# Kernel tuning notes

Hardware: AMD Instinct MI355X
Metric: run time of the kernel (lower is better)

The kernel has to match this reference:

```python
import jax, jax.numpy as jnp
import numpy as np

K = 10
ALPHA = 0.1

def setup_inputs() -> dict:
    key = jax.random.key(0)
    k1, k2, k3, k4 = jax.random.split(key, 4)
    N, E, IN, HID, OUT = 100000, 3200000, 512, 256, 64
    x = jax.random.normal(k1, (N, IN), dtype=jnp.float32)
    edge_index = jax.random.randint(k2, (2, E), 0, N, dtype=jnp.int64)
    W1 = jax.random.normal(k3, (IN, HID), dtype=jnp.float32) * (1.0 / np.sqrt(IN))
    b1 = jnp.zeros((HID,), jnp.float32)
    W2 = jax.random.normal(k4, (HID, OUT), dtype=jnp.float32) * (1.0 / np.sqrt(HID))
    b2 = jnp.zeros((OUT,), jnp.float32)
    return {"x": x, "edge_index": edge_index, "W1": W1, "b1": b1, "W2": W2, "b2": b2}

def reference(x, edge_index, W1, b1, W2, b2):
    N = x.shape[0]
    # gcn_norm with self-loops (PyG default for APPNP)
    loop = jnp.arange(N, dtype=edge_index.dtype)
    src = jnp.concatenate([edge_index[0], loop])  # [E+N]
    dst = jnp.concatenate([edge_index[1], loop])
    ones = jnp.ones(src.shape[0], dtype=x.dtype)
    deg = jax.ops.segment_sum(ones, dst, num_segments=N)
    dis = jnp.where(deg > 0, jax.lax.rsqrt(deg), 0.0)
    norm = dis[src] * dis[dst]  # [E+N]

    # 2-layer MLP (dropout disabled: eval mode)
    h = jnp.maximum(x @ W1 + b1, 0.0) @ W2 + b2  # [N, out]

    # K-step PPR diffusion: z <- alpha*h + (1-alpha)*A_hat z
    def step(z, _):
        agg = jax.ops.segment_sum(norm[:, None] * z[src], dst, num_segments=N)
        return ALPHA * h + (1.0 - ALPHA) * agg, None

    z, _ = jax.lax.scan(step, h, None, length=K)
    return jax.nn.log_softmax(z, axis=-1)
```

## Files before the change

kernel.cpp:

```cpp
#include <hip/hip_runtime.h>
#include <hip/hip_bf16.h>

#define ALPHA_F 0.1f
#define KSTEPS 10
#define BKT_SH 9
#define P1_CHUNK 8192
#define MAXPAD_PER_BUCKET (512 * 32)

typedef __attribute__((ext_vector_type(8))) short bf16x8;
typedef __attribute__((ext_vector_type(4))) float f32x4;

__device__ __forceinline__ unsigned short f2bf(float f) {
  union { float f; unsigned int u; } v; v.f = f;
  unsigned int u = v.u;
  u += 0x7FFFu + ((u >> 16) & 1u);
  return (unsigned short)(u >> 16);
}
__device__ __forceinline__ float bflo(unsigned int u) { return __uint_as_float(u << 16); }
__device__ __forceinline__ float bfhi(unsigned int u) { return __uint_as_float(u & 0xFFFF0000u); }

__device__ __forceinline__ void gload16(const void* g, void* l) {
  __builtin_amdgcn_global_load_lds(
      (const __attribute__((address_space(1))) void*)g,
      (__attribute__((address_space(3))) void*)l, 16, 0, 0);
}


__global__ __launch_bounds__(256)
void p0_hist(const int* __restrict__ dstv, int E, int* __restrict__ bhist) {
  __shared__ int h[256];
  int t = threadIdx.x;
  h[t] = 0;
  __syncthreads();
  int b0 = blockIdx.x * P1_CHUNK;
  int lim = min(P1_CHUNK, E - b0);
  for (int i = t; i < lim; i += 256) atomicAdd(&h[dstv[b0 + i] >> BKT_SH], 1);
  __syncthreads();
  if (h[t]) atomicAdd(&bhist[t], h[t]);
}

__global__ void p0_scan(const int* __restrict__ bhist, int* __restrict__ bbase,
                        int* __restrict__ gcur) {
  __shared__ int s[256];
  int t = threadIdx.x;
  int mine = bhist[t];
  s[t] = mine;
  __syncthreads();
  for (int off = 1; off < 256; off <<= 1) {
    int v = (t >= off) ? s[t - off] : 0;
    __syncthreads();
    s[t] += v;
    __syncthreads();
  }
  int excl = s[t] - mine;
  bbase[t] = excl;
  gcur[t] = excl;
}

__global__ __launch_bounds__(256)
void p1_scatter(const int* __restrict__ srcv, const int* __restrict__ dstv, int E,
                int* __restrict__ gcur, int2* __restrict__ tmp) {
  __shared__ int h[256];
  __shared__ int loc[256];
  int t = threadIdx.x;
  int b0 = blockIdx.x * P1_CHUNK;
  int lim = min(P1_CHUNK, E - b0);
  h[t] = 0;
  __syncthreads();
  for (int i = t; i < lim; i += 256) atomicAdd(&h[dstv[b0 + i] >> BKT_SH], 1);
  __syncthreads();
  loc[t] = h[t] ? atomicAdd(&gcur[t], h[t]) : 0;
  __syncthreads();
  h[t] = 0;
  __syncthreads();
  for (int i = t; i < lim; i += 256) {
    int d = dstv[b0 + i], s = srcv[b0 + i];
    int b = d >> BKT_SH;
    int pos = loc[b] + atomicAdd(&h[b], 1);
    tmp[pos] = make_int2(s, d);
  }
}

__global__ __launch_bounds__(256)
void p2_bucket(const int2* __restrict__ tmp, const int* __restrict__ bbase,
               const int* __restrict__ bhist, int* __restrict__ counts,
               int* __restrict__ rowptr, int* __restrict__ col, int N) {
  __shared__ int h1[512];
  __shared__ int cur[512];
  __shared__ int s2[256];
  const int t = threadIdx.x;
  const int b = blockIdx.x;
  const int base = bbase[b];
  const int pbase = base + b * MAXPAD_PER_BUCKET;
  const int sz = bhist[b];
  const int r0 = b << BKT_SH;
  const int nrows = min(512, N - r0);

  h1[t] = 0; h1[t + 256] = 0;
  __syncthreads();
  for (int i = t; i < sz; i += 256) atomicAdd(&h1[tmp[base + i].y - r0], 1);
  __syncthreads();
  int a = (h1[2 * t] + 31) & ~31;
  int c = (h1[2 * t + 1] + 31) & ~31;
  s2[t] = a + c;
  __syncthreads();
  for (int off = 1; off < 256; off <<= 1) {
    int v = (t >= off) ? s2[t - off] : 0;
    __syncthreads();
    s2[t] += v;
    __syncthreads();
  }
  int excl2 = s2[t] - (a + c);
  cur[2 * t] = excl2;
  cur[2 * t + 1] = excl2 + a;
  __syncthreads();
  if (t < nrows)       { rowptr[r0 + t] = pbase + cur[t];             counts[r0 + t] = h1[t]; }
  if (t + 256 < nrows) { rowptr[r0 + t + 256] = pbase + cur[t + 256]; counts[r0 + t + 256] = h1[t + 256]; }
  __syncthreads();
  for (int i = t; i < sz; i += 256) {
    int2 e = tmp[base + i];
    int p = pbase + atomicAdd(&cur[e.y - r0], 1);
    col[p] = e.x;
  }
  __syncthreads();
  for (int i = t; i < nrows; i += 256) {
    int cnt = h1[i];
    int c32 = (cnt + 31) & ~31;
    int ps = pbase + cur[i];
    for (int k = cnt; k < c32; ++k) col[ps++] = N;
  }
}

__global__ void k_dis(const int* __restrict__ counts, float* __restrict__ dis, int N) {
  int i = blockIdx.x * 256 + threadIdx.x;
  if (i < N) dis[i] = rsqrtf((float)(counts[i] + 1));
}

__global__ void k_zrow(unsigned short* __restrict__ yA, unsigned short* __restrict__ yB, int N) {
  int t = threadIdx.x;
  if (t < 64) yA[(size_t)N * 64 + t] = 0;
  else        yB[(size_t)N * 64 + (t - 64)] = 0;
}

__global__ void k_wconv1(const float* __restrict__ W, unsigned short* __restrict__ WT) {
  int idx = blockIdx.x * 256 + threadIdx.x;
  if (idx >= 512 * 256) return;
  int e = idx & 7, n = (idx >> 3) & 15, q = (idx >> 7) & 7;
  int nsub = (idx >> 10) & 15, kstep = idx >> 14;
  int k = kstep * 64 + q * 8 + e;
  int ncol = nsub * 16 + n;
  WT[idx] = f2bf(W[(size_t)k * 256 + ncol]);
}

__global__ void k_wconv2(const float* __restrict__ W, unsigned short* __restrict__ WT) {
  int idx = blockIdx.x * 256 + threadIdx.x;
  if (idx >= 256 * 64) return;
  int e = idx & 7, n = (idx >> 3) & 15, q = (idx >> 7) & 7;
  int nsub = (idx >> 10) & 3, kstep = idx >> 12;
  int k = kstep * 64 + q * 8 + e;
  int ncol = nsub * 16 + n;
  WT[idx] = f2bf(W[(size_t)k * 64 + ncol]);
}

__global__ __launch_bounds__(512)
void gemm1_kernel(const float* __restrict__ X, const unsigned short* __restrict__ Bt,
                  const float* __restrict__ bias, unsigned short* __restrict__ outT,
                  int M) {
  __shared__ __align__(16) unsigned short Al[8192];
  __shared__ __align__(16) unsigned short Bl[16384];
  const int t = threadIdx.x;
  const int m0 = blockIdx.x * 128;
  const int lane = t & 63;
  const int w = t >> 6;
  const int wm = w >> 2, wn = w & 3;

  const int sm = ((t >> 7) << 4) + (t & 15);
  const int sq = (t >> 4) & 7;
  const int r1 = m0 + sm;
  const int r2 = r1 + 64;
  const bool g1 = r1 < M, g2 = r2 < M;

  f32x4 acc[4][4] = {};

  for (int ks = 0; ks < 8; ++ks) {
    const int kc = ks * 64 + sq * 8;
    uint4 v1 = {0, 0, 0, 0}, v2 = {0, 0, 0, 0};
    if (g1) {
      const float* p = X + (size_t)r1 * 512 + kc;
      float4 a = *(const float4*)p, b = *(const float4*)(p + 4);
      unsigned short* o = (unsigned short*)&v1;
      o[0] = f2bf(a.x); o[1] = f2bf(a.y); o[2] = f2bf(a.z); o[3] = f2bf(a.w);
      o[4] = f2bf(b.x); o[5] = f2bf(b.y); o[6] = f2bf(b.z); o[7] = f2bf(b.w);
    }
    if (g2) {
      const float* p = X + (size_t)r2 * 512 + kc;
      float4 a = *(const float4*)p, b = *(const float4*)(p + 4);
      unsigned short* o = (unsigned short*)&v2;
      o[0] = f2bf(a.x); o[1] = f2bf(a.y); o[2] = f2bf(a.z); o[3] = f2bf(a.w);
      o[4] = f2bf(b.x); o[5] = f2bf(b.y); o[6] = f2bf(b.z); o[7] = f2bf(b.w);
    }
    *(uint4*)&Al[t * 8] = v1;
    *(uint4*)&Al[(t + 512) * 8] = v2;

    const unsigned short* bs = Bt + ks * 16384;
    gload16(bs + (size_t)t * 8,          &Bl[t * 8]);
    gload16(bs + (size_t)(t + 512) * 8,  &Bl[(t + 512) * 8]);
    gload16(bs + (size_t)(t + 1024) * 8, &Bl[(t + 1024) * 8]);
    gload16(bs + (size_t)(t + 1536) * 8, &Bl[(t + 1536) * 8]);
    __syncthreads();

#pragma unroll
    for (int kk = 0; kk < 2; ++kk) {
      bf16x8 af[4], bfv[4];
#pragma unroll
      for (int mi = 0; mi < 4; ++mi)
        af[mi] = *(const bf16x8*)&Al[((wm * 4 + mi) * 128 + kk * 64 + (lane >> 4) * 16 + (lane & 15)) * 8];
#pragma unroll
      for (int ni = 0; ni < 4; ++ni)
        bfv[ni] = *(const bf16x8*)&Bl[((wn * 4 + ni) * 128 + kk * 64 + (lane >> 4) * 16 + (lane & 15)) * 8];
#pragma unroll
      for (int mi = 0; mi < 4; ++mi)
#pragma unroll
        for (int ni = 0; ni < 4; ++ni)
          acc[mi][ni] = __builtin_amdgcn_mfma_f32_16x16x32_bf16(af[mi], bfv[ni], acc[mi][ni], 0, 0, 0);
    }
    __syncthreads();
  }

  unsigned short* ob = outT + (size_t)blockIdx.x * 32768;
#pragma unroll
  for (int mi = 0; mi < 4; ++mi) {
#pragma unroll
    for (int ni = 0; ni < 4; ++ni) {
      int n = wn * 64 + ni * 16 + (lane & 15);
      float bv = bias[n];
      int kstep = n >> 6, q = (n >> 3) & 7, e = n & 7;
#pragma unroll
      for (int j = 0; j < 4; ++j) {
        int lm = wm * 64 + mi * 16 + (lane >> 4) * 4 + j;
        if (m0 + lm < M) {
          float v = fmaxf(acc[mi][ni][j] + bv, 0.f);
          int msub = lm >> 4, mm = lm & 15;
          ob[((((kstep * 8 + msub) * 8 + q) * 16 + mm) * 8) + e] = f2bf(v);
        }
      }
    }
  }
}

__global__ __launch_bounds__(256)
void gemm2_kernel(const unsigned short* __restrict__ At, const unsigned short* __restrict__ Bt,
                  const float* __restrict__ bias, const float* __restrict__ dis,
                  unsigned short* __restrict__ hb, unsigned short* __restrict__ y0, int M) {
  __shared__ __align__(16) unsigned short Al[8192];
  __shared__ __align__(16) unsigned short Bl[4096];
  const int t = threadIdx.x;
  const int m0 = blockIdx.x * 128;
  const int lane = t & 63;
  const int w = t >> 6;
  const int wm = w >> 1, wn = w & 1;

  f32x4 acc[4][2] = {};

  const unsigned short* ab = At + (size_t)blockIdx.x * 32768;
  for (int ks = 0; ks < 4; ++ks) {
    const unsigned short* as = ab + ks * 8192;
    gload16(as + (size_t)t * 8,         &Al[t * 8]);
    gload16(as + (size_t)(t + 256) * 8, &Al[(t + 256) * 8]);
    gload16(as + (size_t)(t + 512) * 8, &Al[(t + 512) * 8]);
    gload16(as + (size_t)(t + 768) * 8, &Al[(t + 768) * 8]);
    const unsigned short* bs = Bt + ks * 4096;
    gload16(bs + (size_t)t * 8,         &Bl[t * 8]);
    gload16(bs + (size_t)(t + 256) * 8, &Bl[(t + 256) * 8]);
    __syncthreads();

#pragma unroll
    for (int kk = 0; kk < 2; ++kk) {
      bf16x8 af[4], bfv[2];
#pragma unroll
      for (int mi = 0; mi < 4; ++mi)
        af[mi] = *(const bf16x8*)&Al[((wm * 4 + mi) * 128 + kk * 64 + (lane >> 4) * 16 + (lane & 15)) * 8];
#pragma unroll
      for (int ni = 0; ni < 2; ++ni)
        bfv[ni] = *(const bf16x8*)&Bl[((wn * 2 + ni) * 128 + kk * 64 + (lane >> 4) * 16 + (lane & 15)) * 8];
#pragma unroll
      for (int mi = 0; mi < 4; ++mi)
#pragma unroll
        for (int ni = 0; ni < 2; ++ni)
          acc[mi][ni] = __builtin_amdgcn_mfma_f32_16x16x32_bf16(af[mi], bfv[ni], acc[mi][ni], 0, 0, 0);
    }
    __syncthreads();
  }

#pragma unroll
  for (int mi = 0; mi < 4; ++mi) {
#pragma unroll
    for (int ni = 0; ni < 2; ++ni) {
      int gn = wn * 32 + ni * 16 + (lane & 15);
      float bv = bias[gn];
#pragma unroll
      for (int j = 0; j < 4; ++j) {
        int gm = m0 + wm * 64 + mi * 16 + (lane >> 4) * 4 + j;
        if (gm < M) {
          float v = acc[mi][ni][j] + bv;
          hb[(size_t)gm * 64 + gn] = f2bf(v);
          y0[(size_t)gm * 64 + gn] = f2bf(dis[gm] * v);
        }
      }
    }
  }
}

template<bool FINAL>
__global__ __launch_bounds__(256)
void prop_kernel(const unsigned short* __restrict__ yin,
                 const unsigned short* __restrict__ hb,
                 void* __restrict__ yout,
                 const int* __restrict__ rowptr, const int* __restrict__ counts,
                 const int* __restrict__ col, const float* __restrict__ dis, int N) {
  int wid = (blockIdx.x * 256 + threadIdx.x) >> 6;
  wid = __builtin_amdgcn_readfirstlane(wid);
  if (wid >= N) return;
  const int lane = threadIdx.x & 63;
  const int g = lane >> 3;
  const int lg = lane & 7;
  const int r = wid;

  const int start = rowptr[r];
  const int cnt = counts[r];
  const int iters = (cnt + 31) >> 5;
  const float dr = dis[r];
  uint4 zs = *(const uint4*)(yin + (size_t)r * 64 + 8 * lg);
  uint4 hr = *(const uint4*)(hb + (size_t)r * 64 + 8 * lg);

  float acc[8] = {0.f, 0.f, 0.f, 0.f, 0.f, 0.f, 0.f, 0.f};
  const int* cp = col + start + 4 * g;
  for (int it = 0; it < iters; ++it, cp += 32) {
    int4 cc = *(const int4*)cp;
    uint4 z0 = *(const uint4*)(yin + (size_t)cc.x * 64 + 8 * lg);
    uint4 z1 = *(const uint4*)(yin + (size_t)cc.y * 64 + 8 * lg);
    uint4 z2 = *(const uint4*)(yin + (size_t)cc.z * 64 + 8 * lg);
    uint4 z3 = *(const uint4*)(yin + (size_t)cc.w * 64 + 8 * lg);
    acc[0] += bflo(z0.x); acc[1] += bfhi(z0.x); acc[2] += bflo(z0.y); acc[3] += bfhi(z0.y);
    acc[4] += bflo(z0.z); acc[5] += bfhi(z0.z); acc[6] += bflo(z0.w); acc[7] += bfhi(z0.w);
    acc[0] += bflo(z1.x); acc[1] += bfhi(z1.x); acc[2] += bflo(z1.y); acc[3] += bfhi(z1.y);
    acc[4] += bflo(z1.z); acc[5] += bfhi(z1.z); acc[6] += bflo(z1.w); acc[7] += bfhi(z1.w);
    acc[0] += bflo(z2.x); acc[1] += bfhi(z2.x); acc[2] += bflo(z2.y); acc[3] += bfhi(z2.y);
    acc[4] += bflo(z2.z); acc[5] += bfhi(z2.z); acc[6] += bflo(z2.w); acc[7] += bfhi(z2.w);
    acc[0] += bflo(z3.x); acc[1] += bfhi(z3.x); acc[2] += bflo(z3.y); acc[3] += bfhi(z3.y);
    acc[4] += bflo(z3.z); acc[5] += bfhi(z3.z); acc[6] += bflo(z3.w); acc[7] += bfhi(z3.w);
  }
#pragma unroll
  for (int k = 0; k < 8; ++k) {
    acc[k] += __shfl_xor(acc[k], 8);
    acc[k] += __shfl_xor(acc[k], 16);
    acc[k] += __shfl_xor(acc[k], 32);
  }

  float selfz[8] = { bflo(zs.x), bfhi(zs.x), bflo(zs.y), bfhi(zs.y),
                     bflo(zs.z), bfhi(zs.z), bflo(zs.w), bfhi(zs.w) };
  float hv[8]    = { bflo(hr.x), bfhi(hr.x), bflo(hr.y), bfhi(hr.y),
                     bflo(hr.z), bfhi(hr.z), bflo(hr.w), bfhi(hr.w) };
  float f[8];
#pragma unroll
  for (int k = 0; k < 8; ++k)
    f[k] = ALPHA_F * hv[k] + (1.f - ALPHA_F) * dr * (acc[k] + selfz[k]);

  if (!FINAL) {
    if (g == 0) {
      uint4 o;
      o.x = (unsigned)f2bf(dr * f[0]) | ((unsigned)f2bf(dr * f[1]) << 16);
      o.y = (unsigned)f2bf(dr * f[2]) | ((unsigned)f2bf(dr * f[3]) << 16);
      o.z = (unsigned)f2bf(dr * f[4]) | ((unsigned)f2bf(dr * f[5]) << 16);
      o.w = (unsigned)f2bf(dr * f[6]) | ((unsigned)f2bf(dr * f[7]) << 16);
      *(uint4*)((unsigned short*)yout + (size_t)r * 64 + 8 * lg) = o;
    }
  } else {
    float m = f[0];
#pragma unroll
    for (int k = 1; k < 8; ++k) m = fmaxf(m, f[k]);
    m = fmaxf(m, __shfl_xor(m, 1));
    m = fmaxf(m, __shfl_xor(m, 2));
    m = fmaxf(m, __shfl_xor(m, 4));
    float s = 0.f;
#pragma unroll
    for (int k = 0; k < 8; ++k) s += __expf(f[k] - m);
    s += __shfl_xor(s, 1);
    s += __shfl_xor(s, 2);
    s += __shfl_xor(s, 4);
    float ls = __logf(s);
    if (g == 0) {
      float* op = (float*)yout + (size_t)r * 64 + 8 * lg;
      *(float4*)op       = make_float4(f[0] - m - ls, f[1] - m - ls, f[2] - m - ls, f[3] - m - ls);
      *(float4*)(op + 4) = make_float4(f[4] - m - ls, f[5] - m - ls, f[6] - m - ls, f[7] - m - ls);
    }
  }
}

extern "C" void kernel_launch(void* const* d_in, const int* in_sizes, int n_in,
                              void* d_out, int out_size, void* d_ws, size_t ws_size,
                              hipStream_t stream) {
  const float* x  = (const float*)d_in[0];
  const int*   ei = (const int*)d_in[1];
  const float* W1 = (const float*)d_in[2];
  const float* b1 = (const float*)d_in[3];
  const float* W2 = (const float*)d_in[4];
  const float* b2 = (const float*)d_in[5];

  const int IN = 512, HID = 256, OUT = 64;
  const int N = in_sizes[0] / IN;
  const int E = in_sizes[1] / 2;
  const int* srcv = ei;
  const int* dstv = ei + E;
  const int NBUCK = (N + (1 << BKT_SH) - 1) >> BKT_SH;
  const int MT = (N + 127) / 128;
  const size_t N1 = (size_t)N + 1;

  char* p = (char*)d_ws;
  auto alloc = [&](size_t bytes) -> void* {
    void* r = (void*)p;
    p += (bytes + 255) & ~(size_t)255;
    return r;
  };
  int*   bhist  = (int*)alloc(256 * 4);
  int*   bbase  = (int*)alloc(256 * 4);
  int*   gcur   = (int*)alloc(256 * 4);
  int*   counts = (int*)alloc((size_t)N * 4);
  float* dis    = (float*)alloc((size_t)N * 4);
  int*   rowptr = (int*)alloc((size_t)(N + 1) * 4);
  int*   col    = (int*)alloc(((size_t)E + 256 * MAXPAD_PER_BUCKET) * 4);
  unsigned short* WT1t = (unsigned short*)alloc((size_t)IN * HID * 2);
  unsigned short* WT2t = (unsigned short*)alloc((size_t)HID * OUT * 2);
  unsigned short* hb   = (unsigned short*)alloc((size_t)N * OUT * 2);
  unsigned short* yA   = (unsigned short*)alloc(N1 * OUT * 2);
  size_t hidT_bytes = (size_t)MT * 32768 * 2;
  size_t R_bytes = hidT_bytes;
  if ((size_t)E * 8 > R_bytes) R_bytes = (size_t)E * 8;
  if (N1 * OUT * 2 > R_bytes) R_bytes = N1 * OUT * 2;
  char* R = (char*)alloc(R_bytes);
  int2* tmp = (int2*)R;
  unsigned short* hidT = (unsigned short*)R;
  unsigned short* yB = (unsigned short*)R;

  hipMemsetAsync(bhist, 0, 256 * 4, stream);

  const int p1blocks = (E + P1_CHUNK - 1) / P1_CHUNK;
  p0_hist<<<p1blocks, 256, 0, stream>>>(dstv, E, bhist);
  p0_scan<<<1, 256, 0, stream>>>(bhist, bbase, gcur);
  p1_scatter<<<p1blocks, 256, 0, stream>>>(srcv, dstv, E, gcur, tmp);
  p2_bucket<<<NBUCK, 256, 0, stream>>>(tmp, bbase, bhist, counts, rowptr, col, N);
  k_dis<<<(N + 255) / 256, 256, 0, stream>>>(counts, dis, N);

  k_wconv1<<<(IN * HID + 255) / 256, 256, 0, stream>>>(W1, WT1t);
  k_wconv2<<<(HID * OUT + 255) / 256, 256, 0, stream>>>(W2, WT2t);

  gemm1_kernel<<<MT, 512, 0, stream>>>(x, WT1t, b1, hidT, N);
  gemm2_kernel<<<MT, 256, 0, stream>>>(hidT, WT2t, b2, dis, hb, yA, N);
  k_zrow<<<1, 128, 0, stream>>>(yA, yB, N);

  const int pblocks = (N + 3) / 4;
  const unsigned short* ycur = yA;
  for (int it = 0; it < KSTEPS - 1; ++it) {
    unsigned short* ynext = (it & 1) ? yA : yB;
    prop_kernel<false><<<pblocks, 256, 0, stream>>>(ycur, hb, ynext, rowptr, counts, col, dis, N);
    ycur = ynext;
  }
  prop_kernel<true><<<pblocks, 256, 0, stream>>>(ycur, hb, d_out, rowptr, counts, col, dis, N);
}
```

Before: 764.8 us.

## Pack edge tmp into int, fuse dis into bucket pass, double-buffer gemm1

The edge scatter buffer now packs the source index and the in-bucket destination offset into a single int, which halves the temporary traffic in the p1 and p2 passes. The degree-norm computation moves into p2_bucket, removing a separate kernel launch. gemm1 switches to a 32-wide K step with double-buffered shared memory, and it prefetches the next X tile into registers while MFMAs run on the current one. The packing assumes src < 2^22 and the new gemm loop has more barriers and iterations.

```diff
diff --git a/kernel.cpp b/kernel.cpp
--- a/kernel.cpp
+++ b/kernel.cpp
@@ -59,7 +59,7 @@
 
 __global__ __launch_bounds__(256)
 void p1_scatter(const int* __restrict__ srcv, const int* __restrict__ dstv, int E,
-                int* __restrict__ gcur, int2* __restrict__ tmp) {
+                int* __restrict__ gcur, int* __restrict__ tmp) {
   __shared__ int h[256];
   __shared__ int loc[256];
   int t = threadIdx.x;
@@ -77,14 +77,15 @@
     int d = dstv[b0 + i], s = srcv[b0 + i];
     int b = d >> BKT_SH;
     int pos = loc[b] + atomicAdd(&h[b], 1);
-    tmp[pos] = make_int2(s, d);
+    tmp[pos] = (s << BKT_SH) | (d & 511);
   }
 }
 
 __global__ __launch_bounds__(256)
-void p2_bucket(const int2* __restrict__ tmp, const int* __restrict__ bbase,
+void p2_bucket(const int* __restrict__ tmp, const int* __restrict__ bbase,
                const int* __restrict__ bhist, int* __restrict__ counts,
-               int* __restrict__ rowptr, int* __restrict__ col, int N) {
+               float* __restrict__ dis, int* __restrict__ rowptr,
+               int* __restrict__ col, int N) {
   __shared__ int h1[512];
   __shared__ int cur[512];
   __shared__ int s2[256];
@@ -98,7 +99,7 @@
 
   h1[t] = 0; h1[t + 256] = 0;
   __syncthreads();
-  for (int i = t; i < sz; i += 256) atomicAdd(&h1[tmp[base + i].y - r0], 1);
+  for (int i = t; i < sz; i += 256) atomicAdd(&h1[tmp[base + i] & 511], 1);
   __syncthreads();
   int a = (h1[2 * t] + 31) & ~31;
   int c = (h1[2 * t + 1] + 31) & ~31;
@@ -114,13 +115,21 @@
   cur[2 * t] = excl2;
   cur[2 * t + 1] = excl2 + a;
   __syncthreads();
-  if (t < nrows)       { rowptr[r0 + t] = pbase + cur[t];             counts[r0 + t] = h1[t]; }
-  if (t + 256 < nrows) { rowptr[r0 + t + 256] = pbase + cur[t + 256]; counts[r0 + t + 256] = h1[t + 256]; }
+  if (t < nrows) {
+    rowptr[r0 + t] = pbase + cur[t];
+    counts[r0 + t] = h1[t];
+    dis[r0 + t] = rsqrtf((float)(h1[t] + 1));
+  }
+  if (t + 256 < nrows) {
+    rowptr[r0 + t + 256] = pbase + cur[t + 256];
+    counts[r0 + t + 256] = h1[t + 256];
+    dis[r0 + t + 256] = rsqrtf((float)(h1[t + 256] + 1));
+  }
   __syncthreads();
   for (int i = t; i < sz; i += 256) {
-    int2 e = tmp[base + i];
-    int p = pbase + atomicAdd(&cur[e.y - r0], 1);
-    col[p] = e.x;
+    int u = tmp[base + i];
+    int p = pbase + atomicAdd(&cur[u & 511], 1);
+    col[p] = u >> BKT_SH;
   }
   __syncthreads();
   for (int i = t; i < nrows; i += 256) {
@@ -131,11 +140,6 @@
   }
 }
 
-__global__ void k_dis(const int* __restrict__ counts, float* __restrict__ dis, int N) {
-  int i = blockIdx.x * 256 + threadIdx.x;
-  if (i < N) dis[i] = rsqrtf((float)(counts[i] + 1));
-}
-
 __global__ void k_zrow(unsigned short* __restrict__ yA, unsigned short* __restrict__ yB, int N) {
   int t = threadIdx.x;
   if (t < 64) yA[(size_t)N * 64 + t] = 0;
@@ -145,9 +149,9 @@
 __global__ void k_wconv1(const float* __restrict__ W, unsigned short* __restrict__ WT) {
   int idx = blockIdx.x * 256 + threadIdx.x;
   if (idx >= 512 * 256) return;
-  int e = idx & 7, n = (idx >> 3) & 15, q = (idx >> 7) & 7;
-  int nsub = (idx >> 10) & 15, kstep = idx >> 14;
-  int k = kstep * 64 + q * 8 + e;
+  int e = idx & 7, n = (idx >> 3) & 15, q = (idx >> 7) & 3;
+  int nsub = (idx >> 9) & 15, kstep = idx >> 13;
+  int k = kstep * 32 + q * 8 + e;
   int ncol = nsub * 16 + n;
   WT[idx] = f2bf(W[(size_t)k * 256 + ncol]);
 }
@@ -166,65 +170,73 @@
 void gemm1_kernel(const float* __restrict__ X, const unsigned short* __restrict__ Bt,
                   const float* __restrict__ bias, unsigned short* __restrict__ outT,
                   int M) {
-  __shared__ __align__(16) unsigned short Al[8192];
-  __shared__ __align__(16) unsigned short Bl[16384];
+  __shared__ __align__(16) unsigned short Al[2][4096];
+  __shared__ __align__(16) unsigned short Bl[2][8192];
   const int t = threadIdx.x;
   const int m0 = blockIdx.x * 128;
   const int lane = t & 63;
   const int w = t >> 6;
   const int wm = w >> 2, wn = w & 3;
 
-  const int sm = ((t >> 7) << 4) + (t & 15);
-  const int sq = (t >> 4) & 7;
-  const int r1 = m0 + sm;
-  const int r2 = r1 + 64;
-  const bool g1 = r1 < M, g2 = r2 < M;
+  const int am = t & 15;
+  const int aq = (t >> 4) & 3;
+  const int amsub = t >> 6;
+  const int arow = m0 + amsub * 16 + am;
+  const bool ag = arow < M;
+  const int aoff = amsub * 512 + aq * 128 + am * 8;
 
   f32x4 acc[4][4] = {};
 
-  for (int ks = 0; ks < 8; ++ks) {
-    const int kc = ks * 64 + sq * 8;
-    uint4 v1 = {0, 0, 0, 0}, v2 = {0, 0, 0, 0};
-    if (g1) {
-      const float* p = X + (size_t)r1 * 512 + kc;
+  {
+    uint4 vv = {0, 0, 0, 0};
+    if (ag) {
+      const float* p = X + (size_t)arow * 512 + aq * 8;
       float4 a = *(const float4*)p, b = *(const float4*)(p + 4);
-      unsigned short* o = (unsigned short*)&v1;
+      unsigned short* o = (unsigned short*)&vv;
       o[0] = f2bf(a.x); o[1] = f2bf(a.y); o[2] = f2bf(a.z); o[3] = f2bf(a.w);
       o[4] = f2bf(b.x); o[5] = f2bf(b.y); o[6] = f2bf(b.z); o[7] = f2bf(b.w);
     }
-    if (g2) {
-      const float* p = X + (size_t)r2 * 512 + kc;
-      float4 a = *(const float4*)p, b = *(const float4*)(p + 4);
-      unsigned short* o = (unsigned short*)&v2;
-      o[0] = f2bf(a.x); o[1] = f2bf(a.y); o[2] = f2bf(a.z); o[3] = f2bf(a.w);
-      o[4] = f2bf(b.x); o[5] = f2bf(b.y); o[6] = f2bf(b.z); o[7] = f2bf(b.w);
-    }
-    *(uint4*)&Al[t * 8] = v1;
-    *(uint4*)&Al[(t + 512) * 8] = v2;
-
-    const unsigned short* bs = Bt + ks * 16384;
-    gload16(bs + (size_t)t * 8,          &Bl[t * 8]);
-    gload16(bs + (size_t)(t + 512) * 8,  &Bl[(t + 512) * 8]);
-    gload16(bs + (size_t)(t + 1024) * 8, &Bl[(t + 1024) * 8]);
-    gload16(bs + (size_t)(t + 1536) * 8, &Bl[(t + 1536) * 8]);
-    __syncthreads();
-
-#pragma unroll
-    for (int kk = 0; kk < 2; ++kk) {
-      bf16x8 af[4], bfv[4];
-#pragma unroll
-      for (int mi = 0; mi < 4; ++mi)
-        af[mi] = *(const bf16x8*)&Al[((wm * 4 + mi) * 128 + kk * 64 + (lane >> 4) * 16 + (lane & 15)) * 8];
+    *(uint4*)&Al[0][aoff] = vv;
+    gload16(Bt + (size_t)t * 8,         &Bl[0][t * 8]);
+    gload16(Bt + (size_t)(t + 512) * 8, &Bl[0][(t + 512) * 8]);
+  }
+  __syncthreads();
+
+  int cur = 0;
+  for (int ks = 0; ks < 16; ++ks) {
+    const bool more = ks < 15;
+    float4 xa = {0, 0, 0, 0}, xb = {0, 0, 0, 0};
+    if (more && ag) {
+      const float* p = X + (size_t)arow * 512 + (ks + 1) * 32 + aq * 8;
+      xa = *(const float4*)p;
+      xb = *(const float4*)(p + 4);
+    }
+    bf16x8 af[4], bfv[4];
+#pragma unroll
+    for (int mi = 0; mi < 4; ++mi)
+      af[mi] = *(const bf16x8*)&Al[cur][(((wm * 4 + mi) * 4 + (lane >> 4)) * 16 + (lane & 15)) * 8];
+#pragma unroll
+    for (int ni = 0; ni < 4; ++ni)
+      bfv[ni] = *(const bf16x8*)&Bl[cur][(((wn * 4 + ni) * 4 + (lane >> 4)) * 16 + (lane & 15)) * 8];
+#pragma unroll
+    for (int mi = 0; mi < 4; ++mi)
 #pragma unroll
       for (int ni = 0; ni < 4; ++ni)
-        bfv[ni] = *(const bf16x8*)&Bl[((wn * 4 + ni) * 128 + kk * 64 + (lane >> 4) * 16 + (lane & 15)) * 8];
-#pragma unroll
-      for (int mi = 0; mi < 4; ++mi)
-#pragma unroll
-        for (int ni = 0; ni < 4; ++ni)
-          acc[mi][ni] = __builtin_amdgcn_mfma_f32_16x16x32_bf16(af[mi], bfv[ni], acc[mi][ni], 0, 0, 0);
-    }
-    __syncthreads();
+        acc[mi][ni] = __builtin_amdgcn_mfma_f32_16x16x32_bf16(af[mi], bfv[ni], acc[mi][ni], 0, 0, 0);
+    if (more) {
+      uint4 vv = {0, 0, 0, 0};
+      if (ag) {
+        unsigned short* o = (unsigned short*)&vv;
+        o[0] = f2bf(xa.x); o[1] = f2bf(xa.y); o[2] = f2bf(xa.z); o[3] = f2bf(xa.w);
+        o[4] = f2bf(xb.x); o[5] = f2bf(xb.y); o[6] = f2bf(xb.z); o[7] = f2bf(xb.w);
+      }
+      *(uint4*)&Al[cur ^ 1][aoff] = vv;
+      const unsigned short* bs = Bt + (size_t)(ks + 1) * 8192;
+      gload16(bs + (size_t)t * 8,         &Bl[cur ^ 1][t * 8]);
+      gload16(bs + (size_t)(t + 512) * 8, &Bl[cur ^ 1][(t + 512) * 8]);
+    }
+    __syncthreads();
+    cur ^= 1;
   }
 
   unsigned short* ob = outT + (size_t)blockIdx.x * 32768;
@@ -427,7 +439,7 @@
   int*   gcur   = (int*)alloc(256 * 4);
   int*   counts = (int*)alloc((size_t)N * 4);
   float* dis    = (float*)alloc((size_t)N * 4);
-  int*   rowptr = (int*)alloc((size_t)(N + 1) * 4);
+  int*   rowptr = (int*)alloc((size_t)N * 4);
   int*   col    = (int*)alloc(((size_t)E + 256 * MAXPAD_PER_BUCKET) * 4);
   unsigned short* WT1t = (unsigned short*)alloc((size_t)IN * HID * 2);
   unsigned short* WT2t = (unsigned short*)alloc((size_t)HID * OUT * 2);
@@ -435,10 +447,10 @@
   unsigned short* yA   = (unsigned short*)alloc(N1 * OUT * 2);
   size_t hidT_bytes = (size_t)MT * 32768 * 2;
   size_t R_bytes = hidT_bytes;
-  if ((size_t)E * 8 > R_bytes) R_bytes = (size_t)E * 8;
+  if ((size_t)E * 4 > R_bytes) R_bytes = (size_t)E * 4;
   if (N1 * OUT * 2 > R_bytes) R_bytes = N1 * OUT * 2;
   char* R = (char*)alloc(R_bytes);
-  int2* tmp = (int2*)R;
+  int* tmp = (int*)R;
   unsigned short* hidT = (unsigned short*)R;
   unsigned short* yB = (unsigned short*)R;
 
@@ -448,8 +460,7 @@
   p0_hist<<<p1blocks, 256, 0, stream>>>(dstv, E, bhist);
   p0_scan<<<1, 256, 0, stream>>>(bhist, bbase, gcur);
   p1_scatter<<<p1blocks, 256, 0, stream>>>(srcv, dstv, E, gcur, tmp);
-  p2_bucket<<<NBUCK, 256, 0, stream>>>(tmp, bbase, bhist, counts, rowptr, col, N);
-  k_dis<<<(N + 255) / 256, 256, 0, stream>>>(counts, dis, N);
+  p2_bucket<<<NBUCK, 256, 0, stream>>>(tmp, bbase, bhist, counts, dis, rowptr, col, N);
 
   k_wconv1<<<(IN * HID + 255) / 256, 256, 0, stream>>>(W1, WT1t);
   k_wconv2<<<(HID * OUT + 255) / 256, 256, 0, stream>>>(W2, WT2t);
```

New measurement: 758.7 us, median of 2. About the same (-0.8%).
